# Kernel tuning notes

Measured on AMD Instinct MI355X. Metric: run time of the kernel, lower is better.

Reference implementation:

```python
import jax, jax.numpy as jnp
import numpy as np

B, T, V, H = 2048, 48, 59, 512


def _uniform(key, shape, fan_in):
    stdv = 1.0 / np.sqrt(fan_in)
    return jax.random.uniform(key, shape, jnp.float32, -stdv, stdv)


def setup_inputs() -> dict:
    key = jax.random.key(0)
    ks = jax.random.split(key, 24)
    x = jax.random.normal(ks[0], (B, T, V), jnp.float32)
    mask = (jax.random.uniform(ks[1], (B, T, V)) < 0.8).astype(jnp.float32)
    deltas = jax.random.uniform(ks[2], (B, T, V), jnp.float32)
    return {
        "x": x, "mask": mask, "deltas": deltas,
        # Decay h (temp_decay_h): W [H,V], b [H]
        "W_gh": _uniform(ks[3], (H, V), V), "b_gh": _uniform(ks[4], (H,), V),
        # Decay x (diag): only diagonal of [V,V] is used -> store diag [V]
        "w_gx": _uniform(ks[5], (V,), V), "b_gx": _uniform(ks[6], (V,), V),
        # hist: Linear(H -> V)
        "W_hist": _uniform(ks[7], (V, H), H), "b_hist": _uniform(ks[8], (V,), H),
        "W_fr": _uniform(ks[9], (V, V), V), "b_fr": _uniform(ks[10], (V,), V),
        # weight_combine: Linear(2V -> V)
        "W_wc": _uniform(ks[11], (V, 2 * V), 2 * V), "b_wc": _uniform(ks[12], (V,), 2 * V),
        # LSTMCell(2V -> H), torch gate order i,f,g,o
        "W_ih": _uniform(ks[13], (4 * H, 2 * V), 2 * V),
        "W_hh": _uniform(ks[14], (4 * H, H), H),
        "b_ih": _uniform(ks[15], (4 * H,), H),
        "b_hh": _uniform(ks[16], (4 * H,), H),
    }


def _rits_forward(x, mask, deltas, W_gh, b_gh, w_gx, b_gx, W_hist, b_hist,
                  W_fr, b_fr, W_wc, b_wc, W_ih, W_hh, b_ih, b_hh):
    Bb, Tt, Vv = x.shape
    Hh = W_gh.shape[0]
    offdiag = 1.0 - jnp.eye(Vv, dtype=x.dtype)
    W_fr_m = W_fr * offdiag

    def step(carry, inp):
        h, c, loss = carry
        x_t, m_t, d_t = inp  # each [B, V]
        # temporal decay of hidden state
        gamma_h = jnp.exp(-jax.nn.relu(d_t @ W_gh.T + b_gh))  # [B, H]
        h = h * gamma_h
        # history-based estimate
        x_h = h @ W_hist.T + b_hist  # [B, V]
        x_r = m_t * x_t + (1.0 - m_t) * x_h
        xu = x_r @ W_fr_m.T + b_fr  # [B, V]
        # diagonal input decay
        gamma_x = jnp.exp(-jax.nn.relu(d_t * w_gx + b_gx))  # [B, V]
        # combination weights (note: no sigmoid, faithful to source)
        beta = jnp.concatenate([gamma_x, m_t], axis=-1) @ W_wc.T + b_wc  # [B, V]
        x_comb = beta * xu + (1.0 - beta) * x_h
        loss = loss + jnp.sum(jnp.abs(x_t - x_comb) * m_t) / (jnp.sum(m_t) + 1e-5)
        x_imp_t = m_t * x_t + (1.0 - m_t) * x_comb
        # LSTM cell
        inp_t = jnp.concatenate([x_imp_t, m_t], axis=-1)  # [B, 2V]
        gates = inp_t @ W_ih.T + b_ih + h @ W_hh.T + b_hh  # [B, 4H]
        i_g, f_g, g_g, o_g = jnp.split(gates, 4, axis=-1)
        c = jax.nn.sigmoid(f_g) * c + jax.nn.sigmoid(i_g) * jnp.tanh(g_g)
        h = jax.nn.sigmoid(o_g) * jnp.tanh(c)
        return (h, c, loss), (x_imp_t, h)

    h0 = jnp.zeros((Bb, Hh), x.dtype)
    c0 = jnp.zeros((Bb, Hh), x.dtype)
    loss0 = jnp.zeros((), x.dtype)
    xs = (jnp.swapaxes(x, 0, 1), jnp.swapaxes(mask, 0, 1), jnp.swapaxes(deltas, 0, 1))
    (h, c, x_loss), (x_imp_t, hiddens_t) = jax.lax.scan(step, (h0, c0, loss0), xs)
    x_imp = jnp.swapaxes(x_imp_t, 0, 1)      # [B, T, V]
    hiddens = jnp.swapaxes(hiddens_t, 0, 1)  # [B, T, H]
    return x_imp, x_loss, hiddens


def reference(x, mask, deltas, W_gh, b_gh, w_gx, b_gx, W_hist, b_hist,
              W_fr, b_fr, W_wc, b_wc, W_ih, W_hh, b_ih, b_hh):
    return _rits_forward(x, mask, deltas, W_gh, b_gh, w_gx, b_gx, W_hist, b_hist,
                         W_fr, b_fr, W_wc, b_wc, W_ih, W_hh, b_ih, b_hh)
```

## Files before the change

### kernel.cpp

```cpp
#include <hip/hip_runtime.h>

#define B_ 2048
#define T_ 48
#define V_ 59
#define H_ 512
#define KP_ 640
#define G4_ 2048

typedef __bf16 bf16x8 __attribute__((ext_vector_type(8)));
typedef float f32x4 __attribute__((ext_vector_type(4)));

__device__ __forceinline__ unsigned short f2bf(float x){
  union { float f; unsigned u; } v; v.f = x;
  unsigned r = (v.u + 0x7FFFu + ((v.u >> 16) & 1u)) >> 16;
  return (unsigned short)r;
}
__device__ __forceinline__ float sigf(float x){ return 1.f/(1.f+expf(-x)); }

static const size_t OFF_Hws = 0;
static const size_t OFF_Cws = 4194304;
static const size_t OFF_LN  = 8388608;
static const size_t OFF_LD  = OFF_LN + 256;
static const size_t MEMSET_BYTES = OFF_LN + 512;
static const size_t OFF_A   = OFF_LN + 512;
static const size_t OFF_WGT = OFF_A  + (size_t)B_*KP_*2;
static const size_t OFF_WGH = OFF_WGT + (size_t)G4_*KP_*2;
static const size_t OFF_WHI = OFF_WGH + (size_t)V_*H_*4;
static const size_t OFF_WFR = OFF_WHI + (size_t)H_*V_*4;
static const size_t OFF_WWC = OFF_WFR + 14080;

__global__ void init_k(const float* __restrict__ W_gh, const float* __restrict__ W_hist,
                       const float* __restrict__ W_fr, const float* __restrict__ W_wc,
                       const float* __restrict__ W_ih, const float* __restrict__ W_hh,
                       float* __restrict__ WghT, float* __restrict__ WhistT,
                       float* __restrict__ WfrT, float* __restrict__ WwcT,
                       unsigned short* __restrict__ WgT)
{
  int tid = blockIdx.x*blockDim.x + threadIdx.x;
  int nt  = gridDim.x*blockDim.x;
  for (int i = tid; i < V_*H_; i += nt){ int v = i >> 9, j = i & 511; WghT[i] = W_gh[j*V_ + v]; }
  for (int i = tid; i < H_*V_; i += nt){ int j = i / V_, v = i - j*V_; WhistT[i] = W_hist[v*H_ + j]; }
  for (int i = tid; i < V_*V_; i += nt){ int u = i / V_, v = i - u*V_; WfrT[i] = (u==v) ? 0.f : W_fr[v*V_ + u]; }
  for (int i = tid; i < 2*V_*V_; i += nt){ int u = i / V_, v = i - u*V_; WwcT[i] = W_wc[v*(2*V_) + u]; }
  for (int i = tid; i < G4_*KP_; i += nt){
    int n = i / KP_, k = i - n*KP_;
    float v = 0.f;
    if (k < 2*V_)      v = W_ih[n*(2*V_) + k];
    else if (k < 630)  v = W_hh[n*H_ + (k-118)];
    WgT[i] = f2bf(v);
  }
}

__global__ __launch_bounds__(512) void phase1(int t,
    const float* __restrict__ x, const float* __restrict__ mk, const float* __restrict__ dl,
    const float* __restrict__ b_gh, const float* __restrict__ w_gx, const float* __restrict__ b_gx,
    const float* __restrict__ b_hist, const float* __restrict__ b_fr, const float* __restrict__ b_wc,
    const float* __restrict__ WghT, const float* __restrict__ WhistT,
    const float* __restrict__ WfrT, const float* __restrict__ WwcT,
    const float* __restrict__ h_ws, unsigned short* __restrict__ A_buf,
    float* __restrict__ out_ximp, float* __restrict__ loss_num, float* __restrict__ loss_den)
{
  __shared__ float d_s[8*64], m_s[8*64], x_s[8*64];
  __shared__ float hs[8*H_];
  __shared__ float xh_s[8*64], xr_s[8*64], gx_s[8*64];
  __shared__ float red[16];
  const int tid = threadIdx.x;
  const int r0  = blockIdx.x * 8;

  if (tid < 8*V_) {
    int b = tid / V_, v = tid - b*V_;
    size_t g = ((size_t)(r0+b)*T_ + t)*V_ + v;
    d_s[b*64+v] = dl[g];
    m_s[b*64+v] = mk[g];
    x_s[b*64+v] = x[g];
  }
  __syncthreads();

  {
    int j = tid;
    float acc[8];
#pragma unroll
    for (int b=0;b<8;++b) acc[b]=0.f;
    for (int v=0; v<V_; ++v) {
      float wv = WghT[v*H_ + j];
#pragma unroll
      for (int b=0;b<8;++b) acc[b] += d_s[b*64+v]*wv;
    }
    float bg = b_gh[j];
#pragma unroll
    for (int b=0;b<8;++b) {
      float gh = expf(-fmaxf(acc[b]+bg, 0.f));
      float hv = h_ws[(size_t)(r0+b)*H_ + j] * gh;
      hs[b*H_+j] = hv;
      A_buf[(size_t)(r0+b)*KP_ + 118 + j] = f2bf(hv);
    }
  }
  if (tid < 128) { int b = tid>>4, p = tid&15; if (p < 10) A_buf[(size_t)(r0+b)*KP_ + 630 + p] = 0; }
  __syncthreads();

  {
    int b = tid>>6, v = tid&63;
    if (v < V_) {
      const float* hp = &hs[b*H_];
      float a0=0.f,a1=0.f,a2=0.f,a3=0.f;
      for (int j=0;j<H_;j+=4){
        a0 += hp[j  ]*WhistT[(j  )*V_+v];
        a1 += hp[j+1]*WhistT[(j+1)*V_+v];
        a2 += hp[j+2]*WhistT[(j+2)*V_+v];
        a3 += hp[j+3]*WhistT[(j+3)*V_+v];
      }
      float xh = b_hist[v] + ((a0+a1)+(a2+a3));
      float mm = m_s[b*64+v], xx = x_s[b*64+v], dd = d_s[b*64+v];
      xh_s[b*64+v] = xh;
      xr_s[b*64+v] = mm*xx + (1.f-mm)*xh;
      gx_s[b*64+v] = expf(-fmaxf(dd*w_gx[v]+b_gx[v], 0.f));
      A_buf[(size_t)(r0+b)*KP_ + V_ + v] = f2bf(mm);
    }
  }
  __syncthreads();

  float num = 0.f, den = 0.f;
  {
    int b = tid>>6, v = tid&63;
    if (v < V_) {
      float xu = b_fr[v], bt = b_wc[v];
      for (int u=0; u<V_; ++u) {
        xu += xr_s[b*64+u]*WfrT[u*V_+v];
        bt += gx_s[b*64+u]*WwcT[u*V_+v] + m_s[b*64+u]*WwcT[(V_+u)*V_+v];
      }
      float xh = xh_s[b*64+v];
      float xc = bt*xu + (1.f-bt)*xh;
      float mm = m_s[b*64+v], xx = x_s[b*64+v];
      num = fabsf(xx - xc)*mm;
      den = mm;
      float xi = mm*xx + (1.f-mm)*xc;
      out_ximp[((size_t)(r0+b)*T_ + t)*V_ + v] = xi;
      A_buf[(size_t)(r0+b)*KP_ + v] = f2bf(xi);
    }
  }
#pragma unroll
  for (int off=32; off; off>>=1){ num += __shfl_down(num, off); den += __shfl_down(den, off); }
  int wid = tid>>6, lane = tid&63;
  if (lane == 0){ red[wid] = num; red[8+wid] = den; }
  __syncthreads();
  if (tid == 0){
    float n=0.f, d=0.f;
    for (int i=0;i<8;++i){ n += red[i]; d += red[8+i]; }
    atomicAdd(&loss_num[t], n);
    atomicAdd(&loss_den[t], d);
  }
}

__global__ __launch_bounds__(256) void phase2(int t,
    const unsigned short* __restrict__ A_buf, const unsigned short* __restrict__ WgT,
    const float* __restrict__ b_ih, const float* __restrict__ b_hh,
    float* __restrict__ h_ws, float* __restrict__ c_ws, float* __restrict__ out_hid)
{
  __shared__ unsigned short ldsA[128*72];
  __shared__ unsigned short ldsB[128*72];
  const int tid  = threadIdx.x;
  const int r0   = blockIdx.x * 128;
  const int j0   = blockIdx.y * 32;
  const int w    = tid >> 6;
  const int lane = tid & 63;
  const int col  = lane & 15;
  const int quad = lane >> 4;

  f32x4 acc[2][8];
#pragma unroll
  for (int i=0;i<2;++i)
#pragma unroll
    for (int j=0;j<8;++j) acc[i][j] = (f32x4)(0.f);

  for (int s = 0; s < 10; ++s) {
#pragma unroll
    for (int p=0; p<4; ++p) {
      int cid = p*256 + tid;
      int row = cid >> 3, c8 = cid & 7;
      uint4 va = *reinterpret_cast<const uint4*>(A_buf + (size_t)(r0+row)*KP_ + s*64 + c8*8);
      *reinterpret_cast<uint4*>(&ldsA[row*72 + c8*8]) = va;
      int ng = ((row>>5)<<9) + j0 + (row&31);
      uint4 vb = *reinterpret_cast<const uint4*>(WgT + (size_t)ng*KP_ + s*64 + c8*8);
      *reinterpret_cast<uint4*>(&ldsB[row*72 + c8*8]) = vb;
    }
    __syncthreads();
#pragma unroll
    for (int kk=0; kk<2; ++kk) {
      bf16x8 af[2], bfr[8];
#pragma unroll
      for (int mf=0; mf<2; ++mf)
        af[mf] = *reinterpret_cast<const bf16x8*>(&ldsA[(w*32 + mf*16 + col)*72 + kk*32 + quad*8]);
#pragma unroll
      for (int nf=0; nf<8; ++nf)
        bfr[nf] = *reinterpret_cast<const bf16x8*>(&ldsB[(nf*16 + col)*72 + kk*32 + quad*8]);
#pragma unroll
      for (int mf=0; mf<2; ++mf)
#pragma unroll
        for (int nf=0; nf<8; ++nf)
          acc[mf][nf] = __builtin_amdgcn_mfma_f32_16x16x32_bf16(af[mf], bfr[nf], acc[mf][nf], 0, 0, 0);
    }
    __syncthreads();
  }

#pragma unroll
  for (int uh=0; uh<2; ++uh) {
    int u = j0 + uh*16 + col;
    float bi = b_ih[u]        + b_hh[u];
    float bf_ = b_ih[H_+u]    + b_hh[H_+u];
    float bg = b_ih[2*H_+u]   + b_hh[2*H_+u];
    float bo = b_ih[3*H_+u]   + b_hh[3*H_+u];
#pragma unroll
    for (int mf=0; mf<2; ++mf) {
#pragma unroll
      for (int r=0; r<4; ++r) {
        int b = r0 + w*32 + mf*16 + quad*4 + r;
        float gi = acc[mf][0+uh][r] + bi;
        float gf = acc[mf][2+uh][r] + bf_;
        float gg = acc[mf][4+uh][r] + bg;
        float go = acc[mf][6+uh][r] + bo;
        size_t idx = (size_t)b*H_ + u;
        float co = c_ws[idx];
        float cn = sigf(gf)*co + sigf(gi)*tanhf(gg);
        float hn = sigf(go)*tanhf(cn);
        c_ws[idx] = cn;
        h_ws[idx] = hn;
        out_hid[((size_t)b*T_ + t)*H_ + u] = hn;
      }
    }
  }
}

__global__ void loss_k(const float* __restrict__ loss_num, const float* __restrict__ loss_den,
                       float* __restrict__ out_loss)
{
  int tid = threadIdx.x;
  float v = 0.f;
  if (tid < T_) v = loss_num[tid]/(loss_den[tid] + 1e-5f);
#pragma unroll
  for (int off=32; off; off>>=1) v += __shfl_down(v, off);
  if (tid == 0) *out_loss = v;
}

extern "C" void kernel_launch(void* const* d_in, const int* in_sizes, int n_in,
                              void* d_out, int out_size, void* d_ws, size_t ws_size,
                              hipStream_t stream)
{
  const float* x      = (const float*)d_in[0];
  const float* mk     = (const float*)d_in[1];
  const float* dl     = (const float*)d_in[2];
  const float* W_gh   = (const float*)d_in[3];
  const float* b_gh   = (const float*)d_in[4];
  const float* w_gx   = (const float*)d_in[5];
  const float* b_gx   = (const float*)d_in[6];
  const float* W_hist = (const float*)d_in[7];
  const float* b_hist = (const float*)d_in[8];
  const float* W_fr   = (const float*)d_in[9];
  const float* b_fr   = (const float*)d_in[10];
  const float* W_wc   = (const float*)d_in[11];
  const float* b_wc   = (const float*)d_in[12];
  const float* W_ih   = (const float*)d_in[13];
  const float* W_hh   = (const float*)d_in[14];
  const float* b_ih   = (const float*)d_in[15];
  const float* b_hh   = (const float*)d_in[16];

  char* ws = (char*)d_ws;
  float*          h_ws   = (float*)(ws + OFF_Hws);
  float*          c_ws   = (float*)(ws + OFF_Cws);
  float*          lnum   = (float*)(ws + OFF_LN);
  float*          lden   = (float*)(ws + OFF_LD);
  unsigned short* A_buf  = (unsigned short*)(ws + OFF_A);
  unsigned short* WgT    = (unsigned short*)(ws + OFF_WGT);
  float*          WghT   = (float*)(ws + OFF_WGH);
  float*          WhistT = (float*)(ws + OFF_WHI);
  float*          WfrT   = (float*)(ws + OFF_WFR);
  float*          WwcT   = (float*)(ws + OFF_WWC);

  float* out      = (float*)d_out;
  float* out_ximp = out;
  float* out_loss = out + (size_t)B_*T_*V_;
  float* out_hid  = out + (size_t)B_*T_*V_ + 1;

  hipMemsetAsync(d_ws, 0, MEMSET_BYTES, stream);
  init_k<<<1024, 256, 0, stream>>>(W_gh, W_hist, W_fr, W_wc, W_ih, W_hh,
                                   WghT, WhistT, WfrT, WwcT, WgT);
  for (int t = 0; t < T_; ++t) {
    phase1<<<256, 512, 0, stream>>>(t, x, mk, dl, b_gh, w_gx, b_gx, b_hist, b_fr, b_wc,
                                    WghT, WhistT, WfrT, WwcT, h_ws, A_buf,
                                    out_ximp, lnum, lden);
    phase2<<<dim3(16,16), 256, 0, stream>>>(t, A_buf, WgT, b_ih, b_hh,
                                            h_ws, c_ws, out_hid);
  }
  loss_k<<<1, 64, 0, stream>>>(lnum, lden, out_loss);
}
```

Baseline: 2.949 ms.

## Fuse per-timestep kernels into one persistent kernel with grid-wide barriers

Replaces the memset, the init kernel, 96 per-timestep phase1/phase2 launches and the loss kernel with a single persistent kernel of 256 blocks. Blocks are kept in step by atomic-counter grid barriers with one counter slot per phase. Weight transposition, workspace zeroing and the final loss reduction now run inside this kernel. The aim is to remove launch overhead and the gaps between kernels in the sequential recurrence. In exchange it relies on all 256 blocks being co-resident and pays spin-barrier latency; the MFMA wave tiling and LDS padding are also rearranged for 512-thread blocks.

```diff
diff --git a/kernel.cpp b/kernel.cpp
--- a/kernel.cpp
+++ b/kernel.cpp
@@ -6,6 +6,9 @@
 #define H_ 512
 #define KP_ 640
 #define G4_ 2048
+#define NB_ 256
+#define NT_ 512
+#define LDB_ 80
 
 typedef __bf16 bf16x8 __attribute__((ext_vector_type(8)));
 typedef float f32x4 __attribute__((ext_vector_type(4)));
@@ -21,224 +24,268 @@
 static const size_t OFF_Cws = 4194304;
 static const size_t OFF_LN  = 8388608;
 static const size_t OFF_LD  = OFF_LN + 256;
-static const size_t MEMSET_BYTES = OFF_LN + 512;
 static const size_t OFF_A   = OFF_LN + 512;
 static const size_t OFF_WGT = OFF_A  + (size_t)B_*KP_*2;
 static const size_t OFF_WGH = OFF_WGT + (size_t)G4_*KP_*2;
-static const size_t OFF_WHI = OFF_WGH + (size_t)V_*H_*4;
-static const size_t OFF_WFR = OFF_WHI + (size_t)H_*V_*4;
+static const size_t OFF_WHI = OFF_WGH + 120832;
+static const size_t OFF_WFR = OFF_WHI + 120832;
 static const size_t OFF_WWC = OFF_WFR + 14080;
-
-__global__ void init_k(const float* __restrict__ W_gh, const float* __restrict__ W_hist,
-                       const float* __restrict__ W_fr, const float* __restrict__ W_wc,
-                       const float* __restrict__ W_ih, const float* __restrict__ W_hh,
-                       float* __restrict__ WghT, float* __restrict__ WhistT,
-                       float* __restrict__ WfrT, float* __restrict__ WwcT,
-                       unsigned short* __restrict__ WgT)
-{
-  int tid = blockIdx.x*blockDim.x + threadIdx.x;
-  int nt  = gridDim.x*blockDim.x;
-  for (int i = tid; i < V_*H_; i += nt){ int v = i >> 9, j = i & 511; WghT[i] = W_gh[j*V_ + v]; }
-  for (int i = tid; i < H_*V_; i += nt){ int j = i / V_, v = i - j*V_; WhistT[i] = W_hist[v*H_ + j]; }
-  for (int i = tid; i < V_*V_; i += nt){ int u = i / V_, v = i - u*V_; WfrT[i] = (u==v) ? 0.f : W_fr[v*V_ + u]; }
-  for (int i = tid; i < 2*V_*V_; i += nt){ int u = i / V_, v = i - u*V_; WwcT[i] = W_wc[v*(2*V_) + u]; }
-  for (int i = tid; i < G4_*KP_; i += nt){
-    int n = i / KP_, k = i - n*KP_;
-    float v = 0.f;
-    if (k < 2*V_)      v = W_ih[n*(2*V_) + k];
-    else if (k < 630)  v = W_hh[n*H_ + (k-118)];
-    WgT[i] = f2bf(v);
-  }
-}
-
-__global__ __launch_bounds__(512) void phase1(int t,
-    const float* __restrict__ x, const float* __restrict__ mk, const float* __restrict__ dl,
-    const float* __restrict__ b_gh, const float* __restrict__ w_gx, const float* __restrict__ b_gx,
-    const float* __restrict__ b_hist, const float* __restrict__ b_fr, const float* __restrict__ b_wc,
-    const float* __restrict__ WghT, const float* __restrict__ WhistT,
-    const float* __restrict__ WfrT, const float* __restrict__ WwcT,
-    const float* __restrict__ h_ws, unsigned short* __restrict__ A_buf,
-    float* __restrict__ out_ximp, float* __restrict__ loss_num, float* __restrict__ loss_den)
-{
-  __shared__ float d_s[8*64], m_s[8*64], x_s[8*64];
-  __shared__ float hs[8*H_];
-  __shared__ float xh_s[8*64], xr_s[8*64], gx_s[8*64];
-  __shared__ float red[16];
-  const int tid = threadIdx.x;
-  const int r0  = blockIdx.x * 8;
-
-  if (tid < 8*V_) {
-    int b = tid / V_, v = tid - b*V_;
-    size_t g = ((size_t)(r0+b)*T_ + t)*V_ + v;
-    d_s[b*64+v] = dl[g];
-    m_s[b*64+v] = mk[g];
-    x_s[b*64+v] = x[g];
+static const size_t OFF_BAR = OFF_WWC + 28160;
+
+__device__ __forceinline__ void gbar(unsigned* bar, int slot){
+  __syncthreads();
+  if (threadIdx.x == 0){
+    __threadfence();
+    __hip_atomic_fetch_add(&bar[slot], 1u, __ATOMIC_RELEASE, __HIP_MEMORY_SCOPE_AGENT);
+    while (__hip_atomic_load(&bar[slot], __ATOMIC_ACQUIRE, __HIP_MEMORY_SCOPE_AGENT) < NB_)
+      __builtin_amdgcn_s_sleep(1);
+    __threadfence();
   }
   __syncthreads();
+}
+
+union SMem {
+  struct {
+    float d[8*64], m[8*64], x[8*64];
+    float xh[8*64], xr[8*64], gx[8*64];
+    float hs[8*H_];
+    float red[16];
+  } p1;
+  struct {
+    unsigned short A[128*LDB_];
+    unsigned short Bt[128*LDB_];
+  } p2;
+};
+
+__global__ __launch_bounds__(NT_, 2) void rits_fused(
+    const float* __restrict__ x, const float* __restrict__ mk, const float* __restrict__ dl,
+    const float* __restrict__ W_gh, const float* __restrict__ b_gh,
+    const float* __restrict__ w_gx, const float* __restrict__ b_gx,
+    const float* __restrict__ W_hist, const float* __restrict__ b_hist,
+    const float* __restrict__ W_fr, const float* __restrict__ b_fr,
+    const float* __restrict__ W_wc, const float* __restrict__ b_wc,
+    const float* __restrict__ W_ih, const float* __restrict__ W_hh,
+    const float* __restrict__ b_ih, const float* __restrict__ b_hh,
+    char* __restrict__ ws,
+    float* __restrict__ out_ximp, float* __restrict__ out_loss, float* __restrict__ out_hid)
+{
+  float*          h_ws   = (float*)(ws + OFF_Hws);
+  float*          c_ws   = (float*)(ws + OFF_Cws);
+  float*          lnum   = (float*)(ws + OFF_LN);
+  float*          lden   = (float*)(ws + OFF_LD);
+  unsigned short* A_buf  = (unsigned short*)(ws + OFF_A);
+  unsigned short* WgT    = (unsigned short*)(ws + OFF_WGT);
+  float*          WghT   = (float*)(ws + OFF_WGH);
+  float*          WhistT = (float*)(ws + OFF_WHI);
+  float*          WfrT   = (float*)(ws + OFF_WFR);
+  float*          WwcT   = (float*)(ws + OFF_WWC);
+  unsigned*       bar    = (unsigned*)(ws + OFF_BAR);
+
+  __shared__ SMem sm;
+
+  const int tid = threadIdx.x;
+  const int bid = blockIdx.x;
+
+  const int x8 = bid & 7;
+  const int kb = bid >> 3;
+  const int rt = x8*2 + (kb & 1);
+  const int ct = kb >> 1;
+  const int r0 = rt * 128;
+  const int j0 = ct * 32;
+  const int r1 = rt*128 + ct*8;
 
   {
-    int j = tid;
-    float acc[8];
-#pragma unroll
-    for (int b=0;b<8;++b) acc[b]=0.f;
-    for (int v=0; v<V_; ++v) {
-      float wv = WghT[v*H_ + j];
-#pragma unroll
-      for (int b=0;b<8;++b) acc[b] += d_s[b*64+v]*wv;
+    int gt = bid*NT_ + tid;
+    const int nt = NB_*NT_;
+    for (int i = gt; i < V_*H_; i += nt){ int v = i >> 9, j = i & 511; WghT[i] = W_gh[j*V_ + v]; }
+    for (int i = gt; i < H_*V_; i += nt){ int j = i / V_, v = i - j*V_; WhistT[i] = W_hist[v*H_ + j]; }
+    for (int i = gt; i < V_*V_; i += nt){ int u = i / V_, v = i - u*V_; WfrT[i] = (u==v) ? 0.f : W_fr[v*V_ + u]; }
+    for (int i = gt; i < 2*V_*V_; i += nt){ int u = i / V_, v = i - u*V_; WwcT[i] = W_wc[v*(2*V_) + u]; }
+    for (int i = gt; i < G4_*KP_; i += nt){
+      int n = i / KP_, k = i - n*KP_;
+      float v = 0.f;
+      if (k < 2*V_)      v = W_ih[n*(2*V_) + k];
+      else if (k < 630)  v = W_hh[n*H_ + (k-118)];
+      WgT[i] = f2bf(v);
     }
-    float bg = b_gh[j];
-#pragma unroll
-    for (int b=0;b<8;++b) {
-      float gh = expf(-fmaxf(acc[b]+bg, 0.f));
-      float hv = h_ws[(size_t)(r0+b)*H_ + j] * gh;
-      hs[b*H_+j] = hv;
-      A_buf[(size_t)(r0+b)*KP_ + 118 + j] = f2bf(hv);
+    for (int i = gt; i < 2*B_*H_; i += nt) ((float*)ws)[i] = 0.f;
+    for (int i = gt; i < 2*T_;    i += nt) lnum[i] = 0.f;
+    if (gt < T_) { lnum[gt] = 0.f; lden[gt] = 0.f; }
+    for (int i = gt; i < B_*10; i += nt){
+      int b = i / 10, p = i - b*10;
+      A_buf[(size_t)b*KP_ + 630 + p] = 0;
     }
   }
-  if (tid < 128) { int b = tid>>4, p = tid&15; if (p < 10) A_buf[(size_t)(r0+b)*KP_ + 630 + p] = 0; }
-  __syncthreads();
-
-  {
-    int b = tid>>6, v = tid&63;
-    if (v < V_) {
-      const float* hp = &hs[b*H_];
-      float a0=0.f,a1=0.f,a2=0.f,a3=0.f;
-      for (int j=0;j<H_;j+=4){
-        a0 += hp[j  ]*WhistT[(j  )*V_+v];
-        a1 += hp[j+1]*WhistT[(j+1)*V_+v];
-        a2 += hp[j+2]*WhistT[(j+2)*V_+v];
-        a3 += hp[j+3]*WhistT[(j+3)*V_+v];
-      }
-      float xh = b_hist[v] + ((a0+a1)+(a2+a3));
-      float mm = m_s[b*64+v], xx = x_s[b*64+v], dd = d_s[b*64+v];
-      xh_s[b*64+v] = xh;
-      xr_s[b*64+v] = mm*xx + (1.f-mm)*xh;
-      gx_s[b*64+v] = expf(-fmaxf(dd*w_gx[v]+b_gx[v], 0.f));
-      A_buf[(size_t)(r0+b)*KP_ + V_ + v] = f2bf(mm);
+  gbar(bar, 0);
+
+  for (int t = 0; t < T_; ++t) {
+    {
+      if (tid < 8*V_) {
+        int b = tid / V_, v = tid - b*V_;
+        size_t g = ((size_t)(r1+b)*T_ + t)*V_ + v;
+        sm.p1.d[b*64+v] = dl[g];
+        sm.p1.m[b*64+v] = mk[g];
+        sm.p1.x[b*64+v] = x[g];
+      }
+      __syncthreads();
+
+      {
+        int j = tid;
+        float acc[8];
+#pragma unroll
+        for (int b=0;b<8;++b) acc[b]=0.f;
+        for (int v=0; v<V_; ++v) {
+          float wv = WghT[v*H_ + j];
+#pragma unroll
+          for (int b=0;b<8;++b) acc[b] += sm.p1.d[b*64+v]*wv;
+        }
+        float bg = b_gh[j];
+#pragma unroll
+        for (int b=0;b<8;++b) {
+          float gh = expf(-fmaxf(acc[b]+bg, 0.f));
+          float hv = h_ws[(size_t)(r1+b)*H_ + j] * gh;
+          sm.p1.hs[b*H_+j] = hv;
+          A_buf[(size_t)(r1+b)*KP_ + 118 + j] = f2bf(hv);
+        }
+      }
+      __syncthreads();
+
+      {
+        int b = tid>>6, v = tid&63;
+        if (v < V_) {
+          const float4* hp4 = (const float4*)&sm.p1.hs[b*H_];
+          float a0=0.f,a1=0.f,a2=0.f,a3=0.f;
+          for (int j4=0;j4<H_/4;++j4){
+            float4 h4 = hp4[j4];
+            int j = j4*4;
+            a0 += h4.x*WhistT[(j  )*V_+v];
+            a1 += h4.y*WhistT[(j+1)*V_+v];
+            a2 += h4.z*WhistT[(j+2)*V_+v];
+            a3 += h4.w*WhistT[(j+3)*V_+v];
+          }
+          float xh = b_hist[v] + ((a0+a1)+(a2+a3));
+          float mm = sm.p1.m[b*64+v], xx = sm.p1.x[b*64+v], dd = sm.p1.d[b*64+v];
+          sm.p1.xh[b*64+v] = xh;
+          sm.p1.xr[b*64+v] = mm*xx + (1.f-mm)*xh;
+          sm.p1.gx[b*64+v] = expf(-fmaxf(dd*w_gx[v]+b_gx[v], 0.f));
+          A_buf[(size_t)(r1+b)*KP_ + V_ + v] = f2bf(mm);
+        }
+      }
+      __syncthreads();
+
+      float num = 0.f, den = 0.f;
+      {
+        int b = tid>>6, v = tid&63;
+        if (v < V_) {
+          float xu = b_fr[v], bt = b_wc[v];
+          for (int u=0; u<V_; ++u) {
+            xu += sm.p1.xr[b*64+u]*WfrT[u*V_+v];
+            bt += sm.p1.gx[b*64+u]*WwcT[u*V_+v] + sm.p1.m[b*64+u]*WwcT[(V_+u)*V_+v];
+          }
+          float xh = sm.p1.xh[b*64+v];
+          float xc = bt*xu + (1.f-bt)*xh;
+          float mm = sm.p1.m[b*64+v], xx = sm.p1.x[b*64+v];
+          num = fabsf(xx - xc)*mm;
+          den = mm;
+          float xi = mm*xx + (1.f-mm)*xc;
+          out_ximp[((size_t)(r1+b)*T_ + t)*V_ + v] = xi;
+          A_buf[(size_t)(r1+b)*KP_ + v] = f2bf(xi);
+        }
+      }
+#pragma unroll
+      for (int off=32; off; off>>=1){ num += __shfl_down(num, off); den += __shfl_down(den, off); }
+      int wid = tid>>6, lane = tid&63;
+      if (lane == 0){ sm.p1.red[wid] = num; sm.p1.red[8+wid] = den; }
+      __syncthreads();
+      if (tid == 0){
+        float n=0.f, d=0.f;
+        for (int i=0;i<8;++i){ n += sm.p1.red[i]; d += sm.p1.red[8+i]; }
+        atomicAdd(&lnum[t], n);
+        atomicAdd(&lden[t], d);
+      }
     }
+    gbar(bar, 1 + 2*t);
+
+    {
+      const int w    = tid >> 6;
+      const int rg   = w >> 1;
+      const int uh   = w & 1;
+      const int lane = tid & 63;
+      const int col  = lane & 15;
+      const int quad = lane >> 4;
+
+      f32x4 acc[2][4];
+#pragma unroll
+      for (int i=0;i<2;++i)
+#pragma unroll
+        for (int g=0;g<4;++g) acc[i][g] = (f32x4)(0.f);
+
+      for (int s = 0; s < 10; ++s) {
+#pragma unroll
+        for (int p=0; p<2; ++p) {
+          int idx = p*NT_ + tid;
+          int row = idx >> 3, c8 = idx & 7;
+          uint4 va = *reinterpret_cast<const uint4*>(A_buf + (size_t)(r0+row)*KP_ + s*64 + c8*8);
+          *reinterpret_cast<uint4*>(&sm.p2.A[row*LDB_ + c8*8]) = va;
+          int ng = ((row>>5)<<9) + j0 + (row&31);
+          uint4 vb = *reinterpret_cast<const uint4*>(WgT + (size_t)ng*KP_ + s*64 + c8*8);
+          *reinterpret_cast<uint4*>(&sm.p2.Bt[row*LDB_ + c8*8]) = vb;
+        }
+        __syncthreads();
+#pragma unroll
+        for (int kk=0; kk<2; ++kk) {
+          bf16x8 af[2], bfr[4];
+#pragma unroll
+          for (int mf=0; mf<2; ++mf)
+            af[mf] = *reinterpret_cast<const bf16x8*>(&sm.p2.A[(rg*32 + mf*16 + col)*LDB_ + kk*32 + quad*8]);
+#pragma unroll
+          for (int g=0; g<4; ++g)
+            bfr[g] = *reinterpret_cast<const bf16x8*>(&sm.p2.Bt[(g*32 + uh*16 + col)*LDB_ + kk*32 + quad*8]);
+#pragma unroll
+          for (int mf=0; mf<2; ++mf)
+#pragma unroll
+            for (int g=0; g<4; ++g)
+              acc[mf][g] = __builtin_amdgcn_mfma_f32_16x16x32_bf16(af[mf], bfr[g], acc[mf][g], 0, 0, 0);
+        }
+        __syncthreads();
+      }
+
+      {
+        int u = j0 + uh*16 + col;
+        float bi  = b_ih[u]        + b_hh[u];
+        float bf_ = b_ih[H_+u]     + b_hh[H_+u];
+        float bg  = b_ih[2*H_+u]   + b_hh[2*H_+u];
+        float bo  = b_ih[3*H_+u]   + b_hh[3*H_+u];
+#pragma unroll
+        for (int mf=0; mf<2; ++mf) {
+#pragma unroll
+          for (int r=0; r<4; ++r) {
+            int b = r0 + rg*32 + mf*16 + quad*4 + r;
+            float gi = acc[mf][0][r] + bi;
+            float gf = acc[mf][1][r] + bf_;
+            float gg = acc[mf][2][r] + bg;
+            float go = acc[mf][3][r] + bo;
+            size_t idx = (size_t)b*H_ + u;
+            float co = c_ws[idx];
+            float cn = sigf(gf)*co + sigf(gi)*tanhf(gg);
+            float hn = sigf(go)*tanhf(cn);
+            c_ws[idx] = cn;
+            h_ws[idx] = hn;
+            out_hid[((size_t)b*T_ + t)*H_ + u] = hn;
+          }
+        }
+      }
+    }
+    gbar(bar, 2 + 2*t);
   }
-  __syncthreads();
-
-  float num = 0.f, den = 0.f;
-  {
-    int b = tid>>6, v = tid&63;
-    if (v < V_) {
-      float xu = b_fr[v], bt = b_wc[v];
-      for (int u=0; u<V_; ++u) {
-        xu += xr_s[b*64+u]*WfrT[u*V_+v];
-        bt += gx_s[b*64+u]*WwcT[u*V_+v] + m_s[b*64+u]*WwcT[(V_+u)*V_+v];
-      }
-      float xh = xh_s[b*64+v];
-      float xc = bt*xu + (1.f-bt)*xh;
-      float mm = m_s[b*64+v], xx = x_s[b*64+v];
-      num = fabsf(xx - xc)*mm;
-      den = mm;
-      float xi = mm*xx + (1.f-mm)*xc;
-      out_ximp[((size_t)(r0+b)*T_ + t)*V_ + v] = xi;
-      A_buf[(size_t)(r0+b)*KP_ + v] = f2bf(xi);
-    }
+
+  if (bid == 0 && tid < 64) {
+    float v = 0.f;
+    if (tid < T_) v = lnum[tid]/(lden[tid] + 1e-5f);
+#pragma unroll
+    for (int off=32; off; off>>=1) v += __shfl_down(v, off);
+    if (tid == 0) *out_loss = v;
   }
-#pragma unroll
-  for (int off=32; off; off>>=1){ num += __shfl_down(num, off); den += __shfl_down(den, off); }
-  int wid = tid>>6, lane = tid&63;
-  if (lane == 0){ red[wid] = num; red[8+wid] = den; }
-  __syncthreads();
-  if (tid == 0){
-    float n=0.f, d=0.f;
-    for (int i=0;i<8;++i){ n += red[i]; d += red[8+i]; }
-    atomicAdd(&loss_num[t], n);
-    atomicAdd(&loss_den[t], d);
-  }
-}
-
-__global__ __launch_bounds__(256) void phase2(int t,
-    const unsigned short* __restrict__ A_buf, const unsigned short* __restrict__ WgT,
-    const float* __restrict__ b_ih, const float* __restrict__ b_hh,
-    float* __restrict__ h_ws, float* __restrict__ c_ws, float* __restrict__ out_hid)
-{
-  __shared__ unsigned short ldsA[128*72];
-  __shared__ unsigned short ldsB[128*72];
-  const int tid  = threadIdx.x;
-  const int r0   = blockIdx.x * 128;
-  const int j0   = blockIdx.y * 32;
-  const int w    = tid >> 6;
-  const int lane = tid & 63;
-  const int col  = lane & 15;
-  const int quad = lane >> 4;
-
-  f32x4 acc[2][8];
-#pragma unroll
-  for (int i=0;i<2;++i)
-#pragma unroll
-    for (int j=0;j<8;++j) acc[i][j] = (f32x4)(0.f);
-
-  for (int s = 0; s < 10; ++s) {
-#pragma unroll
-    for (int p=0; p<4; ++p) {
-      int cid = p*256 + tid;
-      int row = cid >> 3, c8 = cid & 7;
-      uint4 va = *reinterpret_cast<const uint4*>(A_buf + (size_t)(r0+row)*KP_ + s*64 + c8*8);
-      *reinterpret_cast<uint4*>(&ldsA[row*72 + c8*8]) = va;
-      int ng = ((row>>5)<<9) + j0 + (row&31);
-      uint4 vb = *reinterpret_cast<const uint4*>(WgT + (size_t)ng*KP_ + s*64 + c8*8);
-      *reinterpret_cast<uint4*>(&ldsB[row*72 + c8*8]) = vb;
-    }
-    __syncthreads();
-#pragma unroll
-    for (int kk=0; kk<2; ++kk) {
-      bf16x8 af[2], bfr[8];
-#pragma unroll
-      for (int mf=0; mf<2; ++mf)
-        af[mf] = *reinterpret_cast<const bf16x8*>(&ldsA[(w*32 + mf*16 + col)*72 + kk*32 + quad*8]);
-#pragma unroll
-      for (int nf=0; nf<8; ++nf)
-        bfr[nf] = *reinterpret_cast<const bf16x8*>(&ldsB[(nf*16 + col)*72 + kk*32 + quad*8]);
-#pragma unroll
-      for (int mf=0; mf<2; ++mf)
-#pragma unroll
-        for (int nf=0; nf<8; ++nf)
-          acc[mf][nf] = __builtin_amdgcn_mfma_f32_16x16x32_bf16(af[mf], bfr[nf], acc[mf][nf], 0, 0, 0);
-    }
-    __syncthreads();
-  }
-
-#pragma unroll
-  for (int uh=0; uh<2; ++uh) {
-    int u = j0 + uh*16 + col;
-    float bi = b_ih[u]        + b_hh[u];
-    float bf_ = b_ih[H_+u]    + b_hh[H_+u];
-    float bg = b_ih[2*H_+u]   + b_hh[2*H_+u];
-    float bo = b_ih[3*H_+u]   + b_hh[3*H_+u];
-#pragma unroll
-    for (int mf=0; mf<2; ++mf) {
-#pragma unroll
-      for (int r=0; r<4; ++r) {
-        int b = r0 + w*32 + mf*16 + quad*4 + r;
-        float gi = acc[mf][0+uh][r] + bi;
-        float gf = acc[mf][2+uh][r] + bf_;
-        float gg = acc[mf][4+uh][r] + bg;
-        float go = acc[mf][6+uh][r] + bo;
-        size_t idx = (size_t)b*H_ + u;
-        float co = c_ws[idx];
-        float cn = sigf(gf)*co + sigf(gi)*tanhf(gg);
-        float hn = sigf(go)*tanhf(cn);
-        c_ws[idx] = cn;
-        h_ws[idx] = hn;
-        out_hid[((size_t)b*T_ + t)*H_ + u] = hn;
-      }
-    }
-  }
-}
-
-__global__ void loss_k(const float* __restrict__ loss_num, const float* __restrict__ loss_den,
-                       float* __restrict__ out_loss)
-{
-  int tid = threadIdx.x;
-  float v = 0.f;
-  if (tid < T_) v = loss_num[tid]/(loss_den[tid] + 1e-5f);
-#pragma unroll
-  for (int off=32; off; off>>=1) v += __shfl_down(v, off);
-  if (tid == 0) *out_loss = v;
 }
 
 extern "C" void kernel_launch(void* const* d_in, const int* in_sizes, int n_in,
@@ -264,31 +311,15 @@
   const float* b_hh   = (const float*)d_in[16];
 
   char* ws = (char*)d_ws;
-  float*          h_ws   = (float*)(ws + OFF_Hws);
-  float*          c_ws   = (float*)(ws + OFF_Cws);
-  float*          lnum   = (float*)(ws + OFF_LN);
-  float*          lden   = (float*)(ws + OFF_LD);
-  unsigned short* A_buf  = (unsigned short*)(ws + OFF_A);
-  unsigned short* WgT    = (unsigned short*)(ws + OFF_WGT);
-  float*          WghT   = (float*)(ws + OFF_WGH);
-  float*          WhistT = (float*)(ws + OFF_WHI);
-  float*          WfrT   = (float*)(ws + OFF_WFR);
-  float*          WwcT   = (float*)(ws + OFF_WWC);
-
   float* out      = (float*)d_out;
   float* out_ximp = out;
   float* out_loss = out + (size_t)B_*T_*V_;
   float* out_hid  = out + (size_t)B_*T_*V_ + 1;
 
-  hipMemsetAsync(d_ws, 0, MEMSET_BYTES, stream);
-  init_k<<<1024, 256, 0, stream>>>(W_gh, W_hist, W_fr, W_wc, W_ih, W_hh,
-                                   WghT, WhistT, WfrT, WwcT, WgT);
-  for (int t = 0; t < T_; ++t) {
-    phase1<<<256, 512, 0, stream>>>(t, x, mk, dl, b_gh, w_gx, b_gx, b_hist, b_fr, b_wc,
-                                    WghT, WhistT, WfrT, WwcT, h_ws, A_buf,
-                                    out_ximp, lnum, lden);
-    phase2<<<dim3(16,16), 256, 0, stream>>>(t, A_buf, WgT, b_ih, b_hh,
-                                            h_ws, c_ws, out_hid);
-  }
-  loss_k<<<1, 64, 0, stream>>>(lnum, lden, out_loss);
+  hipMemsetAsync(ws + OFF_BAR, 0, 128*sizeof(unsigned), stream);
+
+  rits_fused<<<NB_, NT_, 0, stream>>>(x, mk, dl, W_gh, b_gh, w_gx, b_gx,
+                                      W_hist, b_hist, W_fr, b_fr, W_wc, b_wc,
+                                      W_ih, W_hh, b_ih, b_hh,
+                                      ws, out_ximp, out_loss, out_hid);
 }
```

Measured after the change: 7.898 ms. +167.8%, slower.

## Use MFMA for history projection and split LSTM GEMM across eight waves

Applied to the files above, without the earlier changes.

In phase1 the per-step h @ W_hist projection moves from a scalar fp32 loop to bf16 MFMA. It reuses the bf16-rounded decayed hidden state staged in LDS, while other threads compute the input decay and mask columns at the same time. Phase2 runs 512 threads per block, each wave taking half the gate columns, and uses an XOR-swizzled unpadded LDS layout to avoid bank conflicts. The zero padding of A_buf moves into the one-time init kernel. The cost is bf16 precision in x_h, which feeds the imputation and the loss.

```diff
diff --git a/kernel.cpp b/kernel.cpp
--- a/kernel.cpp
+++ b/kernel.cpp
@@ -25,21 +25,21 @@
 static const size_t OFF_A   = OFF_LN + 512;
 static const size_t OFF_WGT = OFF_A  + (size_t)B_*KP_*2;
 static const size_t OFF_WGH = OFF_WGT + (size_t)G4_*KP_*2;
-static const size_t OFF_WHI = OFF_WGH + (size_t)V_*H_*4;
-static const size_t OFF_WFR = OFF_WHI + (size_t)H_*V_*4;
+static const size_t OFF_WHB = OFF_WGH + 120832;
+static const size_t OFF_WFR = OFF_WHB + 120832;
 static const size_t OFF_WWC = OFF_WFR + 14080;
 
 __global__ void init_k(const float* __restrict__ W_gh, const float* __restrict__ W_hist,
                        const float* __restrict__ W_fr, const float* __restrict__ W_wc,
                        const float* __restrict__ W_ih, const float* __restrict__ W_hh,
-                       float* __restrict__ WghT, float* __restrict__ WhistT,
+                       float* __restrict__ WghT, unsigned short* __restrict__ WhB,
                        float* __restrict__ WfrT, float* __restrict__ WwcT,
-                       unsigned short* __restrict__ WgT)
+                       unsigned short* __restrict__ WgT, unsigned short* __restrict__ A_buf)
 {
   int tid = blockIdx.x*blockDim.x + threadIdx.x;
   int nt  = gridDim.x*blockDim.x;
   for (int i = tid; i < V_*H_; i += nt){ int v = i >> 9, j = i & 511; WghT[i] = W_gh[j*V_ + v]; }
-  for (int i = tid; i < H_*V_; i += nt){ int j = i / V_, v = i - j*V_; WhistT[i] = W_hist[v*H_ + j]; }
+  for (int i = tid; i < 64*H_; i += nt){ int n = i >> 9; WhB[i] = (n < V_) ? f2bf(W_hist[i]) : (unsigned short)0; }
   for (int i = tid; i < V_*V_; i += nt){ int u = i / V_, v = i - u*V_; WfrT[i] = (u==v) ? 0.f : W_fr[v*V_ + u]; }
   for (int i = tid; i < 2*V_*V_; i += nt){ int u = i / V_, v = i - u*V_; WwcT[i] = W_wc[v*(2*V_) + u]; }
   for (int i = tid; i < G4_*KP_; i += nt){
@@ -49,27 +49,28 @@
     else if (k < 630)  v = W_hh[n*H_ + (k-118)];
     WgT[i] = f2bf(v);
   }
+  for (int i = tid; i < B_*10; i += nt){ int b = i / 10, p = i - b*10; A_buf[(size_t)b*KP_ + 630 + p] = 0; }
 }
 
 __global__ __launch_bounds__(512) void phase1(int t,
     const float* __restrict__ x, const float* __restrict__ mk, const float* __restrict__ dl,
     const float* __restrict__ b_gh, const float* __restrict__ w_gx, const float* __restrict__ b_gx,
     const float* __restrict__ b_hist, const float* __restrict__ b_fr, const float* __restrict__ b_wc,
-    const float* __restrict__ WghT, const float* __restrict__ WhistT,
+    const float* __restrict__ WghT, const unsigned short* __restrict__ WhB,
     const float* __restrict__ WfrT, const float* __restrict__ WwcT,
     const float* __restrict__ h_ws, unsigned short* __restrict__ A_buf,
     float* __restrict__ out_ximp, float* __restrict__ loss_num, float* __restrict__ loss_den)
 {
   __shared__ float d_s[8*64], m_s[8*64], x_s[8*64];
-  __shared__ float hs[8*H_];
   __shared__ float xh_s[8*64], xr_s[8*64], gx_s[8*64];
+  __shared__ unsigned short hA[16*520];
   __shared__ float red[16];
   const int tid = threadIdx.x;
-  const int r0  = blockIdx.x * 8;
+  const int r1  = blockIdx.x * 8;
 
   if (tid < 8*V_) {
     int b = tid / V_, v = tid - b*V_;
-    size_t g = ((size_t)(r0+b)*T_ + t)*V_ + v;
+    size_t g = ((size_t)(r1+b)*T_ + t)*V_ + v;
     d_s[b*64+v] = dl[g];
     m_s[b*64+v] = mk[g];
     x_s[b*64+v] = x[g];
@@ -90,31 +91,47 @@
 #pragma unroll
     for (int b=0;b<8;++b) {
       float gh = expf(-fmaxf(acc[b]+bg, 0.f));
-      float hv = h_ws[(size_t)(r0+b)*H_ + j] * gh;
-      hs[b*H_+j] = hv;
-      A_buf[(size_t)(r0+b)*KP_ + 118 + j] = f2bf(hv);
-    }
-  }
-  if (tid < 128) { int b = tid>>4, p = tid&15; if (p < 10) A_buf[(size_t)(r0+b)*KP_ + 630 + p] = 0; }
+      float hv = h_ws[(size_t)(r1+b)*H_ + j] * gh;
+      unsigned short hb = f2bf(hv);
+      hA[b*520 + j] = hb;
+      A_buf[(size_t)(r1+b)*KP_ + 118 + j] = hb;
+    }
+  }
+  __syncthreads();
+
+  if (tid < 256) {
+    const int w = tid >> 6, lane = tid & 63, col = lane & 15, quad = lane >> 4;
+    f32x4 acc = (f32x4)(0.f);
+    const unsigned short* wb = WhB + (size_t)(w*16 + col)*H_;
+#pragma unroll
+    for (int kk = 0; kk < 16; ++kk) {
+      bf16x8 a  = *reinterpret_cast<const bf16x8*>(&hA[col*520 + kk*32 + quad*8]);
+      bf16x8 bb = *reinterpret_cast<const bf16x8*>(wb + kk*32 + quad*8);
+      acc = __builtin_amdgcn_mfma_f32_16x16x32_bf16(a, bb, acc, 0, 0, 0);
+    }
+    if (quad < 2) {
+      int v = w*16 + col;
+      float bh = (v < V_) ? b_hist[v] : 0.f;
+#pragma unroll
+      for (int r=0; r<4; ++r) xh_s[(quad*4+r)*64 + v] = acc[r] + bh;
+    }
+  } else {
+    for (int i = tid - 256; i < 512; i += 256) {
+      int b = i >> 6, v = i & 63;
+      if (v < V_) {
+        float mm = m_s[b*64+v], dd = d_s[b*64+v];
+        gx_s[b*64+v] = expf(-fmaxf(dd*w_gx[v]+b_gx[v], 0.f));
+        A_buf[(size_t)(r1+b)*KP_ + V_ + v] = f2bf(mm);
+      }
+    }
+  }
   __syncthreads();
 
   {
     int b = tid>>6, v = tid&63;
     if (v < V_) {
-      const float* hp = &hs[b*H_];
-      float a0=0.f,a1=0.f,a2=0.f,a3=0.f;
-      for (int j=0;j<H_;j+=4){
-        a0 += hp[j  ]*WhistT[(j  )*V_+v];
-        a1 += hp[j+1]*WhistT[(j+1)*V_+v];
-        a2 += hp[j+2]*WhistT[(j+2)*V_+v];
-        a3 += hp[j+3]*WhistT[(j+3)*V_+v];
-      }
-      float xh = b_hist[v] + ((a0+a1)+(a2+a3));
-      float mm = m_s[b*64+v], xx = x_s[b*64+v], dd = d_s[b*64+v];
-      xh_s[b*64+v] = xh;
-      xr_s[b*64+v] = mm*xx + (1.f-mm)*xh;
-      gx_s[b*64+v] = expf(-fmaxf(dd*w_gx[v]+b_gx[v], 0.f));
-      A_buf[(size_t)(r0+b)*KP_ + V_ + v] = f2bf(mm);
+      float mm = m_s[b*64+v];
+      xr_s[b*64+v] = mm*x_s[b*64+v] + (1.f-mm)*xh_s[b*64+v];
     }
   }
   __syncthreads();
@@ -134,8 +151,8 @@
       num = fabsf(xx - xc)*mm;
       den = mm;
       float xi = mm*xx + (1.f-mm)*xc;
-      out_ximp[((size_t)(r0+b)*T_ + t)*V_ + v] = xi;
-      A_buf[(size_t)(r0+b)*KP_ + v] = f2bf(xi);
+      out_ximp[((size_t)(r1+b)*T_ + t)*V_ + v] = xi;
+      A_buf[(size_t)(r1+b)*KP_ + v] = f2bf(xi);
     }
   }
 #pragma unroll
@@ -151,73 +168,76 @@
   }
 }
 
-__global__ __launch_bounds__(256) void phase2(int t,
+__global__ __launch_bounds__(512) void phase2(int t,
     const unsigned short* __restrict__ A_buf, const unsigned short* __restrict__ WgT,
     const float* __restrict__ b_ih, const float* __restrict__ b_hh,
     float* __restrict__ h_ws, float* __restrict__ c_ws, float* __restrict__ out_hid)
 {
-  __shared__ unsigned short ldsA[128*72];
-  __shared__ unsigned short ldsB[128*72];
+  __shared__ uint4 ldsA[128*8];
+  __shared__ uint4 ldsB[128*8];
   const int tid  = threadIdx.x;
   const int r0   = blockIdx.x * 128;
   const int j0   = blockIdx.y * 32;
   const int w    = tid >> 6;
+  const int rg   = w >> 1;
+  const int uh   = w & 1;
   const int lane = tid & 63;
   const int col  = lane & 15;
   const int quad = lane >> 4;
 
-  f32x4 acc[2][8];
+  f32x4 acc[2][4];
 #pragma unroll
   for (int i=0;i<2;++i)
 #pragma unroll
-    for (int j=0;j<8;++j) acc[i][j] = (f32x4)(0.f);
+    for (int g=0;g<4;++g) acc[i][g] = (f32x4)(0.f);
 
   for (int s = 0; s < 10; ++s) {
 #pragma unroll
-    for (int p=0; p<4; ++p) {
-      int cid = p*256 + tid;
-      int row = cid >> 3, c8 = cid & 7;
-      uint4 va = *reinterpret_cast<const uint4*>(A_buf + (size_t)(r0+row)*KP_ + s*64 + c8*8);
-      *reinterpret_cast<uint4*>(&ldsA[row*72 + c8*8]) = va;
-      int ng = ((row>>5)<<9) + j0 + (row&31);
-      uint4 vb = *reinterpret_cast<const uint4*>(WgT + (size_t)ng*KP_ + s*64 + c8*8);
-      *reinterpret_cast<uint4*>(&ldsB[row*72 + c8*8]) = vb;
+    for (int p=0; p<2; ++p) {
+      int idx = p*512 + tid;
+      int r = idx >> 3, c = idx & 7;
+      ldsA[r*8 + (c ^ (r&7))] = *reinterpret_cast<const uint4*>(A_buf + (size_t)(r0+r)*KP_ + s*64 + c*8);
+      int ng = ((r>>5)<<9) + j0 + (r&31);
+      ldsB[r*8 + (c ^ (r&7))] = *reinterpret_cast<const uint4*>(WgT + (size_t)ng*KP_ + s*64 + c*8);
     }
     __syncthreads();
 #pragma unroll
     for (int kk=0; kk<2; ++kk) {
-      bf16x8 af[2], bfr[8];
+      bf16x8 af[2], bfr[4];
+#pragma unroll
+      for (int mf=0; mf<2; ++mf) {
+        int r = rg*32 + mf*16 + col;
+        af[mf] = *reinterpret_cast<const bf16x8*>(&ldsA[r*8 + ((kk*4+quad) ^ (r&7))]);
+      }
+#pragma unroll
+      for (int g=0; g<4; ++g) {
+        int r = g*32 + uh*16 + col;
+        bfr[g] = *reinterpret_cast<const bf16x8*>(&ldsB[r*8 + ((kk*4+quad) ^ (r&7))]);
+      }
 #pragma unroll
       for (int mf=0; mf<2; ++mf)
-        af[mf] = *reinterpret_cast<const bf16x8*>(&ldsA[(w*32 + mf*16 + col)*72 + kk*32 + quad*8]);
-#pragma unroll
-      for (int nf=0; nf<8; ++nf)
-        bfr[nf] = *reinterpret_cast<const bf16x8*>(&ldsB[(nf*16 + col)*72 + kk*32 + quad*8]);
-#pragma unroll
-      for (int mf=0; mf<2; ++mf)
-#pragma unroll
-        for (int nf=0; nf<8; ++nf)
-          acc[mf][nf] = __builtin_amdgcn_mfma_f32_16x16x32_bf16(af[mf], bfr[nf], acc[mf][nf], 0, 0, 0);
+#pragma unroll
+        for (int g=0; g<4; ++g)
+          acc[mf][g] = __builtin_amdgcn_mfma_f32_16x16x32_bf16(af[mf], bfr[g], acc[mf][g], 0, 0, 0);
     }
     __syncthreads();
   }
 
-#pragma unroll
-  for (int uh=0; uh<2; ++uh) {
+  {
     int u = j0 + uh*16 + col;
-    float bi = b_ih[u]        + b_hh[u];
-    float bf_ = b_ih[H_+u]    + b_hh[H_+u];
-    float bg = b_ih[2*H_+u]   + b_hh[2*H_+u];
-    float bo = b_ih[3*H_+u]   + b_hh[3*H_+u];
+    float bi  = b_ih[u]        + b_hh[u];
+    float bf_ = b_ih[H_+u]     + b_hh[H_+u];
+    float bg  = b_ih[2*H_+u]   + b_hh[2*H_+u];
+    float bo  = b_ih[3*H_+u]   + b_hh[3*H_+u];
 #pragma unroll
     for (int mf=0; mf<2; ++mf) {
 #pragma unroll
       for (int r=0; r<4; ++r) {
-        int b = r0 + w*32 + mf*16 + quad*4 + r;
-        float gi = acc[mf][0+uh][r] + bi;
-        float gf = acc[mf][2+uh][r] + bf_;
-        float gg = acc[mf][4+uh][r] + bg;
-        float go = acc[mf][6+uh][r] + bo;
+        int b = r0 + rg*32 + mf*16 + quad*4 + r;
+        float gi = acc[mf][0][r] + bi;
+        float gf = acc[mf][1][r] + bf_;
+        float gg = acc[mf][2][r] + bg;
+        float go = acc[mf][3][r] + bo;
         size_t idx = (size_t)b*H_ + u;
         float co = c_ws[idx];
         float cn = sigf(gf)*co + sigf(gi)*tanhf(gg);
@@ -271,7 +291,7 @@
   unsigned short* A_buf  = (unsigned short*)(ws + OFF_A);
   unsigned short* WgT    = (unsigned short*)(ws + OFF_WGT);
   float*          WghT   = (float*)(ws + OFF_WGH);
-  float*          WhistT = (float*)(ws + OFF_WHI);
+  unsigned short* WhB    = (unsigned short*)(ws + OFF_WHB);
   float*          WfrT   = (float*)(ws + OFF_WFR);
   float*          WwcT   = (float*)(ws + OFF_WWC);
 
@@ -282,12 +302,12 @@
 
   hipMemsetAsync(d_ws, 0, MEMSET_BYTES, stream);
   init_k<<<1024, 256, 0, stream>>>(W_gh, W_hist, W_fr, W_wc, W_ih, W_hh,
-                                   WghT, WhistT, WfrT, WwcT, WgT);
+                                   WghT, WhB, WfrT, WwcT, WgT, A_buf);
   for (int t = 0; t < T_; ++t) {
     phase1<<<256, 512, 0, stream>>>(t, x, mk, dl, b_gh, w_gx, b_gx, b_hist, b_fr, b_wc,
-                                    WghT, WhistT, WfrT, WwcT, h_ws, A_buf,
+                                    WghT, WhB, WfrT, WwcT, h_ws, A_buf,
                                     out_ximp, lnum, lden);
-    phase2<<<dim3(16,16), 256, 0, stream>>>(t, A_buf, WgT, b_ih, b_hh,
+    phase2<<<dim3(16,16), 512, 0, stream>>>(t, A_buf, WgT, b_ih, b_hh,
                                             h_ws, c_ws, out_hid);
   }
   loss_k<<<1, 64, 0, stream>>>(lnum, lden, out_loss);
```

New measurement: 2.365 ms. 1.25x faster.
